# Optimization experiments

Measured on AMD Instinct MI355X. Metric: run time of the kernel, lower is better.

Reference implementation:

```python
import jax, jax.numpy as jnp
import numpy as np

H, I, E, K = 1024, 2048, 8, 2
B, T = 4, 2048


def setup_inputs() -> dict:
    key = jax.random.key(0)
    k0, k1, k2, k3 = jax.random.split(key, 4)
    x = jax.random.normal(k0, (B, T, H), dtype=jnp.float32)
    Wg = jax.random.normal(k1, (E, H), dtype=jnp.float32) * 0.02   # gate: Linear(H->E), weight [E,H]
    W1 = jax.random.normal(k2, (E, I, H), dtype=jnp.float32) * 0.02  # per-expert fc1 weights [I,H]
    W2 = jax.random.normal(k3, (E, H, I), dtype=jnp.float32) * 0.02  # per-expert fc2 weights [H,I]
    return {"x": x, "Wg": Wg, "W1": W1, "W2": W2, "top_k": K}


def reference(x, Wg, W1, W2, top_k):
    b, t, h = x.shape
    xf = x.reshape(-1, h)                                  # [N,H], N=B*T
    gate_probs = jax.nn.softmax(xf @ Wg.T, axis=-1)        # [N,E]
    topk_vals, topk_idx = jax.lax.top_k(gate_probs, top_k) # [N,k]
    # Dense all-expert SiLU-MLP (faithful to the original dense MoE):
    hid = jax.nn.silu(jnp.einsum('nh,eih->nei', xf, W1))   # [N,E,I]
    all_outs = jnp.einsum('nei,ehi->neh', hid, W2)         # [N,E,H]
    topk_outs = jnp.take_along_axis(all_outs, topk_idx[:, :, None], axis=1)  # [N,k,H]
    weighted = (topk_outs * topk_vals[:, :, None]).sum(axis=1)               # [N,H]
    return weighted.reshape(b, t, h)
```

## Files before the change

### kernel.cpp

```cpp
#include <hip/hip_runtime.h>
#include <hip/hip_bf16.h>

#define HH 1024
#define II 2048
#define EE 8
#define NTOK 8192
#define NPAIR (NTOK * 2)

typedef __attribute__((ext_vector_type(8))) short bf16x8;
typedef __attribute__((ext_vector_type(4))) float f32x4;
typedef unsigned int u32;

__device__ __forceinline__ ushort f2bf(float f) {
    union { float f; unsigned u; } v; v.f = f;
    unsigned r = v.u + 0x7fffu + ((v.u >> 16) & 1u);
    return (ushort)(r >> 16);
}

__device__ __forceinline__ void gload16(const void* g, void* l) {
    __builtin_amdgcn_global_load_lds((const __attribute__((address_space(1))) u32*)g,
                                     (__attribute__((address_space(3))) u32*)l, 16, 0, 0);
}

__global__ __launch_bounds__(256) void cvt_kernel(const float* __restrict__ src,
                                                  ushort* __restrict__ dst, int n4)
{
    const int i = blockIdx.x * 256 + threadIdx.x;
    if (i >= n4) return;
    const float4 f = ((const float4*)src)[i];
    union { ushort h[4]; uint2 u; } pk;
    pk.h[0] = f2bf(f.x); pk.h[1] = f2bf(f.y); pk.h[2] = f2bf(f.z); pk.h[3] = f2bf(f.w);
    ((uint2*)dst)[i] = pk.u;
}

__global__ __launch_bounds__(256) void gate_kernel(
    const float* __restrict__ x, const float* __restrict__ Wg,
    int* __restrict__ counts, int* __restrict__ tki, float* __restrict__ tkv)
{
    __shared__ int hist[EE];
    const int tid = threadIdx.x;
    if (tid < EE) hist[tid] = 0;
    __syncthreads();

    const int w = tid >> 6, lane = tid & 63;

#pragma unroll 1
    for (int t = 0; t < 8; t++) {
        const int n = blockIdx.x * 32 + w * 8 + t;
        const float* xr = x + (size_t)n * HH;
        float4 xv[4];
#pragma unroll
        for (int c = 0; c < 4; c++) xv[c] = *(const float4*)(xr + c * 256 + lane * 4);

        float dot[EE];
#pragma unroll
        for (int e = 0; e < EE; e++) {
            float s = 0.f;
#pragma unroll
            for (int c = 0; c < 4; c++) {
                const float4 wv = *(const float4*)(Wg + e * HH + c * 256 + lane * 4);
                s += xv[c].x * wv.x + xv[c].y * wv.y + xv[c].z * wv.z + xv[c].w * wv.w;
            }
            for (int off = 32; off > 0; off >>= 1) s += __shfl_down(s, off);
            dot[e] = s;
        }
        if (lane == 0) {
            float m = dot[0];
#pragma unroll
            for (int e = 1; e < EE; e++) m = fmaxf(m, dot[e]);
            float p[EE]; float sum = 0.f;
#pragma unroll
            for (int e = 0; e < EE; e++) { p[e] = __expf(dot[e] - m); sum += p[e]; }
            const float inv = 1.f / sum;
            int i0 = 0; float v0 = p[0];
#pragma unroll
            for (int e = 1; e < EE; e++) if (p[e] > v0) { v0 = p[e]; i0 = e; }
            int i1 = -1; float v1 = -1.f;
#pragma unroll
            for (int e = 0; e < EE; e++) if (e != i0 && p[e] > v1) { v1 = p[e]; i1 = e; }
            tki[n * 2 + 0] = i0; tkv[n * 2 + 0] = v0 * inv;
            tki[n * 2 + 1] = i1; tkv[n * 2 + 1] = v1 * inv;
            atomicAdd(&hist[i0], 1);
            atomicAdd(&hist[i1], 1);
        }
    }
    __syncthreads();
    if (tid < EE) atomicAdd(&counts[tid], hist[tid]);
}

__global__ void offsets_kernel(const int* __restrict__ counts,
                               int* __restrict__ offs, int* __restrict__ cursor)
{
    if (threadIdx.x == 0 && blockIdx.x == 0) {
        int acc = 0;
        for (int e = 0; e < EE; e++) { offs[e] = acc; cursor[e] = acc; acc += counts[e]; }
    }
}

__global__ __launch_bounds__(256) void scatter_kernel(
    const int* __restrict__ tki, const float* __restrict__ tkv,
    int* __restrict__ cursor, int* __restrict__ stok, float* __restrict__ sval)
{
    __shared__ int hist[EE];
    __shared__ int base[EE];
    const int tid = threadIdx.x;
    const int id = blockIdx.x * 256 + tid;
    if (tid < EE) hist[tid] = 0;
    __syncthreads();
    const int e = tki[id];
    const int loc = atomicAdd(&hist[e], 1);
    __syncthreads();
    if (tid < EE) base[tid] = atomicAdd(&cursor[tid], hist[tid]);
    __syncthreads();
    const int p = base[e] + loc;
    stok[p] = id >> 1;
    sval[p] = tkv[id];
}

template <bool PRE>
__global__ __launch_bounds__(256) void fc1_kernel(
    const float* __restrict__ x, const ushort* __restrict__ xb,
    const float* __restrict__ W1, const ushort* __restrict__ W1b,
    const int* __restrict__ counts, const int* __restrict__ offs,
    const int* __restrict__ stok, ushort* __restrict__ hid)
{
    const int e = blockIdx.z;
    const int cnt = counts[e];
    const int row0 = blockIdx.y * 128;
    if (row0 >= cnt) return;
    const int off = offs[e];
    const int col0 = blockIdx.x * 128;

    __shared__ __align__(16) ushort As[128 * 64];
    __shared__ __align__(16) ushort Bs[128 * 64];

    const int tid = threadIdx.x;
    const int w = tid >> 6, lane = tid & 63;
    const int quad = lane >> 4, l16 = lane & 15;
    const int wm = (w >> 1) * 64, wn = (w & 1) * 64;

    f32x4 acc[4][4];
#pragma unroll
    for (int mi = 0; mi < 4; mi++)
#pragma unroll
        for (int ni = 0; ni < 4; ni++) acc[mi][ni] = f32x4{0.f, 0.f, 0.f, 0.f};

    const int sub = lane >> 3;
    const int chk = lane & 7;
    int tokA[4];
    const int fr = tid >> 1;
    const int fc = (tid & 1) * 32;
    int tokF = 0;
    if (PRE) {
#pragma unroll
        for (int i = 0; i < 4; i++) {
            int r = row0 + (w * 4 + i) * 8 + sub;
            if (r >= cnt) r = cnt - 1;
            tokA[i] = stok[off + r];
        }
    } else {
        int r = row0 + fr;
        if (r >= cnt) r = cnt - 1;
        tokF = stok[off + r];
    }

    for (int k0 = 0; k0 < HH; k0 += 64) {
        __syncthreads();
        if (PRE) {
#pragma unroll
            for (int i = 0; i < 4; i++) {
                const ushort* gA = xb + (size_t)tokA[i] * HH + k0 + chk * 8;
                gload16(gA, &As[(w * 4 + i) * 512]);
                const ushort* gB = W1b + ((size_t)e * II + col0 + (w * 4 + i) * 8 + sub) * HH + k0 + chk * 8;
                gload16(gB, &Bs[(w * 4 + i) * 512]);
            }
        } else {
#pragma unroll
            for (int c = 0; c < 32; c += 4) {
                const float4 f = *(const float4*)(x + (size_t)tokF * HH + k0 + fc + c);
                union { ushort h[4]; uint2 u; } pk;
                pk.h[0] = f2bf(f.x); pk.h[1] = f2bf(f.y); pk.h[2] = f2bf(f.z); pk.h[3] = f2bf(f.w);
                *(uint2*)&As[fr * 64 + fc + c] = pk.u;
                const float4 g = *(const float4*)(W1 + ((size_t)e * II + col0 + fr) * HH + k0 + fc + c);
                pk.h[0] = f2bf(g.x); pk.h[1] = f2bf(g.y); pk.h[2] = f2bf(g.z); pk.h[3] = f2bf(g.w);
                *(uint2*)&Bs[fr * 64 + fc + c] = pk.u;
            }
        }
        __syncthreads();

#pragma unroll
        for (int kk = 0; kk < 2; kk++) {
            bf16x8 af[4], bb[4];
#pragma unroll
            for (int mi = 0; mi < 4; mi++)
                af[mi] = *(const bf16x8*)&As[(wm + mi * 16 + l16) * 64 + kk * 32 + quad * 8];
#pragma unroll
            for (int ni = 0; ni < 4; ni++)
                bb[ni] = *(const bf16x8*)&Bs[(wn + ni * 16 + l16) * 64 + kk * 32 + quad * 8];
#pragma unroll
            for (int mi = 0; mi < 4; mi++)
#pragma unroll
                for (int ni = 0; ni < 4; ni++)
                    acc[mi][ni] = __builtin_amdgcn_mfma_f32_16x16x32_bf16(af[mi], bb[ni], acc[mi][ni], 0, 0, 0);
        }
    }

    const int cnt_rem = cnt - row0;
#pragma unroll
    for (int mi = 0; mi < 4; mi++) {
#pragma unroll
        for (int j = 0; j < 4; j++) {
            const int r = wm + mi * 16 + quad * 4 + j;
            if (r < cnt_rem) {
                ushort* hrow = hid + (size_t)(off + row0 + r) * II + col0 + wn + l16;
#pragma unroll
                for (int ni = 0; ni < 4; ni++) {
                    const float v = acc[mi][ni][j];
                    const float s = v / (1.f + __expf(-v));
                    hrow[ni * 16] = f2bf(s);
                }
            }
        }
    }
}

template <bool PRE>
__global__ __launch_bounds__(256) void fc2_kernel(
    const ushort* __restrict__ hid,
    const float* __restrict__ W2, const ushort* __restrict__ W2b,
    const int* __restrict__ counts, const int* __restrict__ offs,
    const int* __restrict__ stok, const float* __restrict__ sval,
    float* __restrict__ out)
{
    const int e = blockIdx.z;
    const int cnt = counts[e];
    const int row0 = blockIdx.y * 128;
    if (row0 >= cnt) return;
    const int off = offs[e];
    const int col0 = blockIdx.x * 128;

    __shared__ __align__(16) ushort As[128 * 64];
    __shared__ __align__(16) ushort Bs[128 * 64];

    const int tid = threadIdx.x;
    const int w = tid >> 6, lane = tid & 63;
    const int quad = lane >> 4, l16 = lane & 15;
    const int wm = (w >> 1) * 64, wn = (w & 1) * 64;

    f32x4 acc[4][4];
#pragma unroll
    for (int mi = 0; mi < 4; mi++)
#pragma unroll
        for (int ni = 0; ni < 4; ni++) acc[mi][ni] = f32x4{0.f, 0.f, 0.f, 0.f};

    const int sub = lane >> 3;
    const int chk = lane & 7;
    size_t slotA[4];
#pragma unroll
    for (int i = 0; i < 4; i++) {
        int s = off + row0 + (w * 4 + i) * 8 + sub;
        if (s > NPAIR - 1) s = NPAIR - 1;
        slotA[i] = (size_t)s;
    }
    const int fr = tid >> 1;
    const int fc = (tid & 1) * 32;

    for (int k0 = 0; k0 < II; k0 += 64) {
        __syncthreads();
#pragma unroll
        for (int i = 0; i < 4; i++) {
            const ushort* gA = hid + slotA[i] * II + k0 + chk * 8;
            gload16(gA, &As[(w * 4 + i) * 512]);
        }
        if (PRE) {
#pragma unroll
            for (int i = 0; i < 4; i++) {
                const ushort* gB = W2b + ((size_t)e * HH + col0 + (w * 4 + i) * 8 + sub) * II + k0 + chk * 8;
                gload16(gB, &Bs[(w * 4 + i) * 512]);
            }
        } else {
#pragma unroll
            for (int c = 0; c < 32; c += 4) {
                const float4 g = *(const float4*)(W2 + ((size_t)e * HH + col0 + fr) * II + k0 + fc + c);
                union { ushort h[4]; uint2 u; } pk;
                pk.h[0] = f2bf(g.x); pk.h[1] = f2bf(g.y); pk.h[2] = f2bf(g.z); pk.h[3] = f2bf(g.w);
                *(uint2*)&Bs[fr * 64 + fc + c] = pk.u;
            }
        }
        __syncthreads();

#pragma unroll
        for (int kk = 0; kk < 2; kk++) {
            bf16x8 af[4], bb[4];
#pragma unroll
            for (int mi = 0; mi < 4; mi++)
                af[mi] = *(const bf16x8*)&As[(wm + mi * 16 + l16) * 64 + kk * 32 + quad * 8];
#pragma unroll
            for (int ni = 0; ni < 4; ni++)
                bb[ni] = *(const bf16x8*)&Bs[(wn + ni * 16 + l16) * 64 + kk * 32 + quad * 8];
#pragma unroll
            for (int mi = 0; mi < 4; mi++)
#pragma unroll
                for (int ni = 0; ni < 4; ni++)
                    acc[mi][ni] = __builtin_amdgcn_mfma_f32_16x16x32_bf16(af[mi], bb[ni], acc[mi][ni], 0, 0, 0);
        }
    }

    const int cnt_rem = cnt - row0;
#pragma unroll
    for (int mi = 0; mi < 4; mi++) {
#pragma unroll
        for (int j = 0; j < 4; j++) {
            const int r = wm + mi * 16 + quad * 4 + j;
            if (r < cnt_rem) {
                const int p = off + row0 + r;
                const int token = stok[p];
                const float val = sval[p];
                float* orow = out + (size_t)token * HH + col0 + wn + l16;
#pragma unroll
                for (int ni = 0; ni < 4; ni++)
                    atomicAdd(&orow[ni * 16], val * acc[mi][ni][j]);
            }
        }
    }
}

extern "C" void kernel_launch(void* const* d_in, const int* in_sizes, int n_in,
                              void* d_out, int out_size, void* d_ws, size_t ws_size,
                              hipStream_t stream) {
    const float* x  = (const float*)d_in[0];
    const float* Wg = (const float*)d_in[1];
    const float* W1 = (const float*)d_in[2];
    const float* W2 = (const float*)d_in[3];
    float* out = (float*)d_out;

    char* wsb = (char*)d_ws;
    int*    counts = (int*)(wsb + 0);
    int*    cursor = (int*)(wsb + 64);
    int*    offs   = (int*)(wsb + 128);
    int*    tki    = (int*)(wsb + 256);
    float*  tkv    = (float*)(wsb + 256 + 65536);
    int*    stok   = (int*)(wsb + 256 + 2 * 65536);
    float*  sval   = (float*)(wsb + 256 + 3 * 65536);
    ushort* hid    = (ushort*)(wsb + 262400);
    ushort* W1b    = (ushort*)(wsb + 262400 + 67108864ull);
    ushort* W2b    = (ushort*)(wsb + 262400 + 100663296ull);
    ushort* xb     = (ushort*)(wsb + 262400 + 134217728ull);
    const size_t REQ = 262400ull + 134217728ull + 16777216ull;
    const bool pre = ws_size >= REQ;

    hipMemsetAsync(wsb, 0, 256, stream);
    hipMemsetAsync(d_out, 0, (size_t)out_size * sizeof(float), stream);

    gate_kernel<<<NTOK / 32, 256, 0, stream>>>(x, Wg, counts, tki, tkv);
    offsets_kernel<<<1, 64, 0, stream>>>(counts, offs, cursor);
    scatter_kernel<<<NPAIR / 256, 256, 0, stream>>>(tki, tkv, cursor, stok, sval);

    if (pre) {
        cvt_kernel<<<(NTOK * HH / 4 + 255) / 256, 256, 0, stream>>>(x, xb, NTOK * HH / 4);
        cvt_kernel<<<(EE * II * HH / 4 + 255) / 256, 256, 0, stream>>>(W1, W1b, EE * II * HH / 4);
        cvt_kernel<<<(EE * HH * II / 4 + 255) / 256, 256, 0, stream>>>(W2, W2b, EE * HH * II / 4);
        fc1_kernel<true><<<dim3(II / 128, NPAIR / 128, EE), 256, 0, stream>>>(x, xb, W1, W1b, counts, offs, stok, hid);
        fc2_kernel<true><<<dim3(HH / 128, NPAIR / 128, EE), 256, 0, stream>>>(hid, W2, W2b, counts, offs, stok, sval, out);
    } else {
        fc1_kernel<false><<<dim3(II / 128, NPAIR / 128, EE), 256, 0, stream>>>(x, xb, W1, W1b, counts, offs, stok, hid);
        fc2_kernel<false><<<dim3(HH / 128, NPAIR / 128, EE), 256, 0, stream>>>(hid, W2, W2b, counts, offs, stok, sval, out);
    }
}
```

Measured before the change: 487.6 us.

## Swizzle LDS tiles with XOR, fuse x conversion into gate, merge weight casts

Applies an XOR swizzle to the 16-byte chunk index in the LDS A/B tiles of both expert GEMMs, so the MFMA fragment reads no longer hit the same banks. The global_load_lds source addresses are permuted to match, and so are the fallback store and read offsets. The gate kernel now also writes the bf16 copy of x, which removes a separate conversion pass over x. The W1 and W2 conversions are merged into one launch. The added cost is extra stores in the gate kernel and some index arithmetic.

```diff
diff --git a/kernel.cpp b/kernel.cpp
--- a/kernel.cpp
+++ b/kernel.cpp
@@ -22,20 +22,23 @@
                                      (__attribute__((address_space(3))) u32*)l, 16, 0, 0);
 }
 
-__global__ __launch_bounds__(256) void cvt_kernel(const float* __restrict__ src,
-                                                  ushort* __restrict__ dst, int n4)
-{
+__global__ __launch_bounds__(256) void cvtw_kernel(
+    const float* __restrict__ W1, const float* __restrict__ W2,
+    ushort* __restrict__ W1b, ushort* __restrict__ W2b)
+{
+    const int N1 = EE * II * HH / 4;
     const int i = blockIdx.x * 256 + threadIdx.x;
-    if (i >= n4) return;
-    const float4 f = ((const float4*)src)[i];
+    const float4 f = (i < N1) ? ((const float4*)W1)[i] : ((const float4*)W2)[i - N1];
     union { ushort h[4]; uint2 u; } pk;
     pk.h[0] = f2bf(f.x); pk.h[1] = f2bf(f.y); pk.h[2] = f2bf(f.z); pk.h[3] = f2bf(f.w);
-    ((uint2*)dst)[i] = pk.u;
+    if (i < N1) ((uint2*)W1b)[i] = pk.u;
+    else        ((uint2*)W2b)[i - N1] = pk.u;
 }
 
 __global__ __launch_bounds__(256) void gate_kernel(
     const float* __restrict__ x, const float* __restrict__ Wg,
-    int* __restrict__ counts, int* __restrict__ tki, float* __restrict__ tkv)
+    int* __restrict__ counts, int* __restrict__ tki, float* __restrict__ tkv,
+    ushort* __restrict__ xb)
 {
     __shared__ int hist[EE];
     const int tid = threadIdx.x;
@@ -51,6 +54,14 @@
         float4 xv[4];
 #pragma unroll
         for (int c = 0; c < 4; c++) xv[c] = *(const float4*)(xr + c * 256 + lane * 4);
+
+#pragma unroll
+        for (int c = 0; c < 4; c++) {
+            union { ushort h[4]; uint2 u; } pk;
+            pk.h[0] = f2bf(xv[c].x); pk.h[1] = f2bf(xv[c].y);
+            pk.h[2] = f2bf(xv[c].z); pk.h[3] = f2bf(xv[c].w);
+            *(uint2*)(xb + (size_t)n * HH + c * 256 + lane * 4) = pk.u;
+        }
 
         float dot[EE];
 #pragma unroll
@@ -138,6 +149,7 @@
     const int w = tid >> 6, lane = tid & 63;
     const int quad = lane >> 4, l16 = lane & 15;
     const int wm = (w >> 1) * 64, wn = (w & 1) * 64;
+    const int l7 = l16 & 7;
 
     f32x4 acc[4][4];
 #pragma unroll
@@ -147,6 +159,7 @@
 
     const int sub = lane >> 3;
     const int chk = lane & 7;
+    const int gchk = chk ^ sub;
     int tokA[4];
     const int fr = tid >> 1;
     const int fc = (tid & 1) * 32;
@@ -169,34 +182,37 @@
         if (PRE) {
 #pragma unroll
             for (int i = 0; i < 4; i++) {
-                const ushort* gA = xb + (size_t)tokA[i] * HH + k0 + chk * 8;
+                const ushort* gA = xb + (size_t)tokA[i] * HH + k0 + gchk * 8;
                 gload16(gA, &As[(w * 4 + i) * 512]);
-                const ushort* gB = W1b + ((size_t)e * II + col0 + (w * 4 + i) * 8 + sub) * HH + k0 + chk * 8;
+                const ushort* gB = W1b + ((size_t)e * II + col0 + (w * 4 + i) * 8 + sub) * HH + k0 + gchk * 8;
                 gload16(gB, &Bs[(w * 4 + i) * 512]);
             }
         } else {
 #pragma unroll
             for (int c = 0; c < 32; c += 4) {
-                const float4 f = *(const float4*)(x + (size_t)tokF * HH + k0 + fc + c);
-                union { ushort h[4]; uint2 u; } pk;
+                const int u = fc + c;
+                const int sw = ((u >> 3) ^ (fr & 7)) * 8 + (u & 7);
+                const float4 f = *(const float4*)(x + (size_t)tokF * HH + k0 + u);
+                union { ushort h[4]; uint2 u2; } pk;
                 pk.h[0] = f2bf(f.x); pk.h[1] = f2bf(f.y); pk.h[2] = f2bf(f.z); pk.h[3] = f2bf(f.w);
-                *(uint2*)&As[fr * 64 + fc + c] = pk.u;
-                const float4 g = *(const float4*)(W1 + ((size_t)e * II + col0 + fr) * HH + k0 + fc + c);
+                *(uint2*)&As[fr * 64 + sw] = pk.u2;
+                const float4 g = *(const float4*)(W1 + ((size_t)e * II + col0 + fr) * HH + k0 + u);
                 pk.h[0] = f2bf(g.x); pk.h[1] = f2bf(g.y); pk.h[2] = f2bf(g.z); pk.h[3] = f2bf(g.w);
-                *(uint2*)&Bs[fr * 64 + fc + c] = pk.u;
+                *(uint2*)&Bs[fr * 64 + sw] = pk.u2;
             }
         }
         __syncthreads();
 
 #pragma unroll
         for (int kk = 0; kk < 2; kk++) {
+            const int pos = ((kk * 4 + quad) ^ l7) * 8;
             bf16x8 af[4], bb[4];
 #pragma unroll
             for (int mi = 0; mi < 4; mi++)
-                af[mi] = *(const bf16x8*)&As[(wm + mi * 16 + l16) * 64 + kk * 32 + quad * 8];
+                af[mi] = *(const bf16x8*)&As[(wm + mi * 16 + l16) * 64 + pos];
 #pragma unroll
             for (int ni = 0; ni < 4; ni++)
-                bb[ni] = *(const bf16x8*)&Bs[(wn + ni * 16 + l16) * 64 + kk * 32 + quad * 8];
+                bb[ni] = *(const bf16x8*)&Bs[(wn + ni * 16 + l16) * 64 + pos];
 #pragma unroll
             for (int mi = 0; mi < 4; mi++)
 #pragma unroll
@@ -246,6 +262,7 @@
     const int w = tid >> 6, lane = tid & 63;
     const int quad = lane >> 4, l16 = lane & 15;
     const int wm = (w >> 1) * 64, wn = (w & 1) * 64;
+    const int l7 = l16 & 7;
 
     f32x4 acc[4][4];
 #pragma unroll
@@ -255,6 +272,7 @@
 
     const int sub = lane >> 3;
     const int chk = lane & 7;
+    const int gchk = chk ^ sub;
     size_t slotA[4];
 #pragma unroll
     for (int i = 0; i < 4; i++) {
@@ -269,35 +287,38 @@
         __syncthreads();
 #pragma unroll
         for (int i = 0; i < 4; i++) {
-            const ushort* gA = hid + slotA[i] * II + k0 + chk * 8;
+            const ushort* gA = hid + slotA[i] * II + k0 + gchk * 8;
             gload16(gA, &As[(w * 4 + i) * 512]);
         }
         if (PRE) {
 #pragma unroll
             for (int i = 0; i < 4; i++) {
-                const ushort* gB = W2b + ((size_t)e * HH + col0 + (w * 4 + i) * 8 + sub) * II + k0 + chk * 8;
+                const ushort* gB = W2b + ((size_t)e * HH + col0 + (w * 4 + i) * 8 + sub) * II + k0 + gchk * 8;
                 gload16(gB, &Bs[(w * 4 + i) * 512]);
             }
         } else {
 #pragma unroll
             for (int c = 0; c < 32; c += 4) {
-                const float4 g = *(const float4*)(W2 + ((size_t)e * HH + col0 + fr) * II + k0 + fc + c);
-                union { ushort h[4]; uint2 u; } pk;
+                const int u = fc + c;
+                const int sw = ((u >> 3) ^ (fr & 7)) * 8 + (u & 7);
+                const float4 g = *(const float4*)(W2 + ((size_t)e * HH + col0 + fr) * II + k0 + u);
+                union { ushort h[4]; uint2 u2; } pk;
                 pk.h[0] = f2bf(g.x); pk.h[1] = f2bf(g.y); pk.h[2] = f2bf(g.z); pk.h[3] = f2bf(g.w);
-                *(uint2*)&Bs[fr * 64 + fc + c] = pk.u;
+                *(uint2*)&Bs[fr * 64 + sw] = pk.u2;
             }
         }
         __syncthreads();
 
 #pragma unroll
         for (int kk = 0; kk < 2; kk++) {
+            const int pos = ((kk * 4 + quad) ^ l7) * 8;
             bf16x8 af[4], bb[4];
 #pragma unroll
             for (int mi = 0; mi < 4; mi++)
-                af[mi] = *(const bf16x8*)&As[(wm + mi * 16 + l16) * 64 + kk * 32 + quad * 8];
+                af[mi] = *(const bf16x8*)&As[(wm + mi * 16 + l16) * 64 + pos];
 #pragma unroll
             for (int ni = 0; ni < 4; ni++)
-                bb[ni] = *(const bf16x8*)&Bs[(wn + ni * 16 + l16) * 64 + kk * 32 + quad * 8];
+                bb[ni] = *(const bf16x8*)&Bs[(wn + ni * 16 + l16) * 64 + pos];
 #pragma unroll
             for (int mi = 0; mi < 4; mi++)
 #pragma unroll
@@ -352,14 +373,12 @@
     hipMemsetAsync(wsb, 0, 256, stream);
     hipMemsetAsync(d_out, 0, (size_t)out_size * sizeof(float), stream);
 
-    gate_kernel<<<NTOK / 32, 256, 0, stream>>>(x, Wg, counts, tki, tkv);
+    gate_kernel<<<NTOK / 32, 256, 0, stream>>>(x, Wg, counts, tki, tkv, xb);
     offsets_kernel<<<1, 64, 0, stream>>>(counts, offs, cursor);
     scatter_kernel<<<NPAIR / 256, 256, 0, stream>>>(tki, tkv, cursor, stok, sval);
 
     if (pre) {
-        cvt_kernel<<<(NTOK * HH / 4 + 255) / 256, 256, 0, stream>>>(x, xb, NTOK * HH / 4);
-        cvt_kernel<<<(EE * II * HH / 4 + 255) / 256, 256, 0, stream>>>(W1, W1b, EE * II * HH / 4);
-        cvt_kernel<<<(EE * HH * II / 4 + 255) / 256, 256, 0, stream>>>(W2, W2b, EE * HH * II / 4);
+        cvtw_kernel<<<(2 * EE * II * HH / 4) / 256, 256, 0, stream>>>(W1, W2, W1b, W2b);
         fc1_kernel<true><<<dim3(II / 128, NPAIR / 128, EE), 256, 0, stream>>>(x, xb, W1, W1b, counts, offs, stok, hid);
         fc2_kernel<true><<<dim3(HH / 128, NPAIR / 128, EE), 256, 0, stream>>>(hid, W2, W2b, counts, offs, stok, sval, out);
     } else {
```

Result: no change. 479.7 us (-1.6%).
